# Performance work log

Hardware: AMD Instinct MI355X
Metric: run time of the kernel (lower is better)

Reference implementation:

```python
import jax, jax.numpy as jnp
import numpy as np

N_OFFSETS = [(1, 0), (1, 1), (0, 1), (-1, 1), (-1, 0), (-1, -1), (0, -1), (1, -1)]
DILATION = 1


def setup_inputs() -> dict:
    key = jax.random.key(0)
    feats = jax.random.normal(key, (8, 128, 256, 256), dtype=jnp.float32)
    return {"feats": feats}


def reference(feats):
    # feats: [B, C, H, W]
    d = DILATION
    B, C, H, W = feats.shape
    # channel-wise L2 normalize (no eps, matching torch .norm division)
    normed = feats / jnp.linalg.norm(feats, axis=1, keepdims=True)
    # reflect pad last two spatial dims by d
    padded = jnp.pad(normed, ((0, 0), (0, 0), (d, d), (d, d)), mode="reflect")
    # 8 shifted multiply + channel-sum correlations (fixed small offset set)
    corrs = jnp.concatenate(
        [
            jnp.sum(
                normed
                * padded[:, :, d - dx * d // d if False else d - dx:H + d - dx, d - dy:W + d - dy],
                axis=1,
                keepdims=True,
            )
            for dx, dy in [(ox * d, oy * d) for ox, oy in N_OFFSETS]
        ],
        axis=1,
    )  # [B, 8, H, W]
    return corrs
```

## Files before the change

kernel.cpp:

```cpp
#include <hip/hip_runtime.h>


#define BB 8
#define CC 128
#define HH 256
#define WW 256
#define CSPLIT 2
#define CPW (CC / CSPLIT)

#define DD(k, j) acc[12 + (k)*4 + (j)]

__global__ __launch_bounds__(128) void featcorr_kernel(
    const float* __restrict__ feats, float* __restrict__ out) {
  const int lane = threadIdx.x;
  const int wy = threadIdx.y;
  const int h = (blockIdx.x % 8) * (HH / 8) + (blockIdx.x / 8);
  const int b = blockIdx.y;

  const int hm = (h == 0) ? 1 : h - 1;
  const int hp = (h == HH - 1) ? HH - 2 : h + 1;

  const size_t HW = (size_t)HH * WW;
  const int col0 = lane * 4;

  const float* pT = feats + ((size_t)b * CC + wy * CPW) * HW + (size_t)hm * WW + col0;
  const float* pM = feats + ((size_t)b * CC + wy * CPW) * HW + (size_t)h * WW + col0;
  const float* pB = feats + ((size_t)b * CC + wy * CPW) * HW + (size_t)hp * WW + col0;

  float acc[44];
#pragma unroll
  for (int a = 0; a < 44; ++a) acc[a] = 0.f;

  auto compute = [&](const float4 t, const float4 m, const float4 bt) {
    const float rT = __shfl_down(t.x, 1);
    const float rM = __shfl_down(m.x, 1);
    const float rB = __shfl_down(bt.x, 1);
    acc[0] += t.x * t.x;  acc[1] += t.y * t.y;  acc[2] += t.z * t.z;  acc[3] += t.w * t.w;
    acc[4] += m.x * m.x;  acc[5] += m.y * m.y;  acc[6] += m.z * m.z;  acc[7] += m.w * m.w;
    acc[8] += bt.x * bt.x; acc[9] += bt.y * bt.y; acc[10] += bt.z * bt.z; acc[11] += bt.w * bt.w;
    DD(0, 0) += m.x * t.x; DD(0, 1) += m.y * t.y; DD(0, 2) += m.z * t.z; DD(0, 3) += m.w * t.w;
    DD(4, 0) += m.x * bt.x; DD(4, 1) += m.y * bt.y; DD(4, 2) += m.z * bt.z; DD(4, 3) += m.w * bt.w;
    DD(1, 1) += m.y * t.x; DD(1, 2) += m.z * t.y; DD(1, 3) += m.w * t.z;
    DD(1, 0) += rM * t.w;
    DD(2, 1) += m.y * m.x; DD(2, 2) += m.z * m.y; DD(2, 3) += m.w * m.z;
    DD(3, 1) += m.y * bt.x; DD(3, 2) += m.z * bt.y; DD(3, 3) += m.w * bt.z;
    DD(3, 0) += rM * bt.w;
    DD(5, 0) += m.x * bt.y; DD(5, 1) += m.y * bt.z; DD(5, 2) += m.z * bt.w; DD(5, 3) += m.w * rB;
    DD(6, 0) += m.x * m.y; DD(6, 1) += m.y * m.z; DD(6, 2) += m.z * m.w; DD(6, 3) += m.w * rM;
    DD(7, 0) += m.x * t.y; DD(7, 1) += m.y * t.z; DD(7, 2) += m.z * t.w; DD(7, 3) += m.w * rT;
  };

#define LOADSTEP(T, M, Bv)        \
  T = *(const float4*)pT;         \
  M = *(const float4*)pM;         \
  Bv = *(const float4*)pB;        \
  pT += HW; pM += HW; pB += HW;

  float4 tA, mA, bA, tB, mB, bB, tC, mC, bC, tD, mD, bD;
  LOADSTEP(tA, mA, bA)
  LOADSTEP(tB, mB, bB)
  LOADSTEP(tC, mC, bC)

  for (int i = 0; i < CPW / 4 - 1; ++i) {
    LOADSTEP(tD, mD, bD) compute(tA, mA, bA);
    LOADSTEP(tA, mA, bA) compute(tB, mB, bB);
    LOADSTEP(tB, mB, bB) compute(tC, mC, bC);
    LOADSTEP(tC, mC, bC) compute(tD, mD, bD);
  }
  LOADSTEP(tD, mD, bD) compute(tA, mA, bA);
  compute(tB, mB, bB);
  compute(tC, mC, bC);
  compute(tD, mD, bD);

  __shared__ float lds[44][64];
  if (wy == 1) {
#pragma unroll
    for (int a = 0; a < 44; ++a) lds[a][lane] = acc[a];
  }
  __syncthreads();

  if (wy == 0) {
#pragma unroll
    for (int a = 0; a < 44; ++a) acc[a] += lds[a][lane];

    const float g1 = __shfl_up(DD(1, 0), 1);
    const float g2 = __shfl_up(DD(6, 3), 1);
    const float g3 = __shfl_up(DD(3, 0), 1);
    DD(1, 0) = (lane == 0) ? DD(7, 0) : g1;
    DD(2, 0) = (lane == 0) ? DD(6, 0) : g2;
    DD(3, 0) = (lane == 0) ? DD(5, 0) : g3;
    if (lane == 63) {
      DD(5, 3) = DD(3, 3);
      DD(6, 3) = DD(2, 3);
      DD(7, 3) = DD(1, 3);
    }

    float it[4], im[4], ib[4];
#pragma unroll
    for (int j = 0; j < 4; ++j) {
      it[j] = rsqrtf(acc[j]);
      im[j] = rsqrtf(acc[4 + j]);
      ib[j] = rsqrtf(acc[8 + j]);
    }
    float IT[6], IM[6], IB[6];
    IT[1] = it[0]; IT[2] = it[1]; IT[3] = it[2]; IT[4] = it[3];
    IM[1] = im[0]; IM[2] = im[1]; IM[3] = im[2]; IM[4] = im[3];
    IB[1] = ib[0]; IB[2] = ib[1]; IB[3] = ib[2]; IB[4] = ib[3];
    const float tl = __shfl_up(it[3], 1), ml = __shfl_up(im[3], 1), bl = __shfl_up(ib[3], 1);
    const float tr = __shfl_down(it[0], 1), mr = __shfl_down(im[0], 1), br = __shfl_down(ib[0], 1);
    IT[0] = (lane == 0) ? it[1] : tl;
    IM[0] = (lane == 0) ? im[1] : ml;
    IB[0] = (lane == 0) ? ib[1] : bl;
    IT[5] = (lane == 63) ? it[2] : tr;
    IM[5] = (lane == 63) ? im[2] : mr;
    IB[5] = (lane == 63) ? ib[2] : br;

    float* obase = out + ((size_t)b * 8) * HW + (size_t)h * WW + col0;
#pragma unroll
    for (int k = 0; k < 8; ++k) {
      float v[4];
#pragma unroll
      for (int j = 0; j < 4; ++j) {
        float in;
        switch (k) {
          case 0: in = it[j];     break;
          case 1: in = IT[j];     break;
          case 2: in = IM[j];     break;
          case 3: in = IB[j];     break;
          case 4: in = ib[j];     break;
          case 5: in = IB[j + 2]; break;
          case 6: in = IM[j + 2]; break;
          default: in = IT[j + 2]; break;
        }
        v[j] = DD(k, j) * im[j] * in;
      }
      float4 o;
      o.x = v[0]; o.y = v[1]; o.z = v[2]; o.w = v[3];
      *(float4*)(obase + (size_t)k * HW) = o;
    }
  }
}

extern "C" void kernel_launch(void* const* d_in, const int* in_sizes, int n_in,
                              void* d_out, int out_size, void* d_ws, size_t ws_size,
                              hipStream_t stream) {
  const float* feats = (const float*)d_in[0];
  float* out = (float*)d_out;
  dim3 block(64, CSPLIT, 1);
  dim3 grid(HH, BB, 1);
  featcorr_kernel<<<grid, block, 0, stream>>>(feats, out);
}
```

Measured before the change: 365.2 us.

## Share row halos across warps via async global-to-LDS multi-buffered pipeline

Each block now handles 4 output rows with one warp per row. The 6 needed input rows per channel are staged into LDS with global_load_lds, using a 10-deep ring buffer controlled by manual vmcnt waits and barriers. The old design split channels across two warps and had each warp load 3 rows directly, so every input row was fetched about three times. Sharing rows across warps cuts that redundant global traffic and removes the cross-warp reduction, at the cost of two barriers per channel and a large LDS footprint (60KB) that limits occupancy.

```diff
diff --git a/kernel.cpp b/kernel.cpp
--- a/kernel.cpp
+++ b/kernel.cpp
@@ -5,33 +5,57 @@
 #define CC 128
 #define HH 256
 #define WW 256
-#define CSPLIT 2
-#define CPW (CC / CSPLIT)
+#define RB 4
+#define NSLOT 6
+#define PD 10
 
 #define DD(k, j) acc[12 + (k)*4 + (j)]
 
-__global__ __launch_bounds__(128) void featcorr_kernel(
+__global__ __launch_bounds__(256) void featcorr_kernel(
     const float* __restrict__ feats, float* __restrict__ out) {
   const int lane = threadIdx.x;
   const int wy = threadIdx.y;
-  const int h = (blockIdx.x % 8) * (HH / 8) + (blockIdx.x / 8);
+  const int rb = blockIdx.x;
   const int b = blockIdx.y;
-
-  const int hm = (h == 0) ? 1 : h - 1;
-  const int hp = (h == HH - 1) ? HH - 2 : h + 1;
+  const int h0 = rb * RB;
+  const int h = h0 + wy;
 
   const size_t HW = (size_t)HH * WW;
   const int col0 = lane * 4;
 
-  const float* pT = feats + ((size_t)b * CC + wy * CPW) * HW + (size_t)hm * WW + col0;
-  const float* pM = feats + ((size_t)b * CC + wy * CPW) * HW + (size_t)h * WW + col0;
-  const float* pB = feats + ((size_t)b * CC + wy * CPW) * HW + (size_t)hp * WW + col0;
+  __shared__ float lds[PD][NSLOT][WW];
+
+  const int hh1 = h0 - 1 + wy;
+  const int sr1 = (hh1 < 0) ? 1 : (hh1 > HH - 1 ? HH - 2 : hh1);
+  const float* p1 = feats + (size_t)b * CC * HW + (size_t)sr1 * WW + col0;
+  const float* p2 = nullptr;
+  if (wy < 2) {
+    const int hh2 = h0 - 1 + (4 + wy);
+    const int sr2 = (hh2 < 0) ? 1 : (hh2 > HH - 1 ? HH - 2 : hh2);
+    p2 = feats + (size_t)b * CC * HW + (size_t)sr2 * WW + col0;
+  }
+
+  auto stage = [&](int buf) {
+    __builtin_amdgcn_global_load_lds(
+        (const __attribute__((address_space(1))) void*)p1,
+        (__attribute__((address_space(3))) void*)&lds[buf][wy][0], 16, 0, 0);
+    p1 += HW;
+    if (wy < 2) {
+      __builtin_amdgcn_global_load_lds(
+          (const __attribute__((address_space(1))) void*)p2,
+          (__attribute__((address_space(3))) void*)&lds[buf][4 + wy][0], 16, 0, 0);
+      p2 += HW;
+    }
+  };
 
   float acc[44];
 #pragma unroll
   for (int a = 0; a < 44; ++a) acc[a] = 0.f;
 
-  auto compute = [&](const float4 t, const float4 m, const float4 bt) {
+  auto compute = [&](int buf) {
+    const float4 t = *(const float4*)&lds[buf][wy][col0];
+    const float4 m = *(const float4*)&lds[buf][wy + 1][col0];
+    const float4 bt = *(const float4*)&lds[buf][wy + 2][col0];
     const float rT = __shfl_down(t.x, 1);
     const float rM = __shfl_down(m.x, 1);
     const float rB = __shfl_down(bt.x, 1);
@@ -50,94 +74,82 @@
     DD(7, 0) += m.x * t.y; DD(7, 1) += m.y * t.z; DD(7, 2) += m.z * t.w; DD(7, 3) += m.w * rT;
   };
 
-#define LOADSTEP(T, M, Bv)        \
-  T = *(const float4*)pT;         \
-  M = *(const float4*)pM;         \
-  Bv = *(const float4*)pB;        \
-  pT += HW; pM += HW; pB += HW;
+#pragma unroll
+  for (int c = 0; c < PD; ++c) stage(c);
 
-  float4 tA, mA, bA, tB, mB, bB, tC, mC, bC, tD, mD, bD;
-  LOADSTEP(tA, mA, bA)
-  LOADSTEP(tB, mB, bB)
-  LOADSTEP(tC, mC, bC)
+  int buf = 0;
+  for (int ch = 0; ch < CC; ++ch) {
+    if (ch < CC - (PD - 1)) {
+      if (wy < 2) {
+        asm volatile("s_waitcnt vmcnt(18)" ::: "memory");
+      } else {
+        asm volatile("s_waitcnt vmcnt(9)" ::: "memory");
+      }
+    } else {
+      asm volatile("s_waitcnt vmcnt(0)" ::: "memory");
+    }
+    asm volatile("s_barrier" ::: "memory");
+    compute(buf);
+    asm volatile("s_waitcnt lgkmcnt(0)" ::: "memory");
+    asm volatile("s_barrier" ::: "memory");
+    if (ch + PD < CC) stage(buf);
+    buf = (buf + 1 == PD) ? 0 : buf + 1;
+  }
 
-  for (int i = 0; i < CPW / 4 - 1; ++i) {
-    LOADSTEP(tD, mD, bD) compute(tA, mA, bA);
-    LOADSTEP(tA, mA, bA) compute(tB, mB, bB);
-    LOADSTEP(tB, mB, bB) compute(tC, mC, bC);
-    LOADSTEP(tC, mC, bC) compute(tD, mD, bD);
+  const float g1 = __shfl_up(DD(1, 0), 1);
+  const float g2 = __shfl_up(DD(6, 3), 1);
+  const float g3 = __shfl_up(DD(3, 0), 1);
+  DD(1, 0) = (lane == 0) ? DD(7, 0) : g1;
+  DD(2, 0) = (lane == 0) ? DD(6, 0) : g2;
+  DD(3, 0) = (lane == 0) ? DD(5, 0) : g3;
+  if (lane == 63) {
+    DD(5, 3) = DD(3, 3);
+    DD(6, 3) = DD(2, 3);
+    DD(7, 3) = DD(1, 3);
   }
-  LOADSTEP(tD, mD, bD) compute(tA, mA, bA);
-  compute(tB, mB, bB);
-  compute(tC, mC, bC);
-  compute(tD, mD, bD);
 
-  __shared__ float lds[44][64];
-  if (wy == 1) {
+  float it[4], im[4], ib[4];
 #pragma unroll
-    for (int a = 0; a < 44; ++a) lds[a][lane] = acc[a];
+  for (int j = 0; j < 4; ++j) {
+    it[j] = rsqrtf(acc[j]);
+    im[j] = rsqrtf(acc[4 + j]);
+    ib[j] = rsqrtf(acc[8 + j]);
   }
-  __syncthreads();
+  float IT[6], IM[6], IB[6];
+  IT[1] = it[0]; IT[2] = it[1]; IT[3] = it[2]; IT[4] = it[3];
+  IM[1] = im[0]; IM[2] = im[1]; IM[3] = im[2]; IM[4] = im[3];
+  IB[1] = ib[0]; IB[2] = ib[1]; IB[3] = ib[2]; IB[4] = ib[3];
+  const float tl = __shfl_up(it[3], 1), ml = __shfl_up(im[3], 1), bl = __shfl_up(ib[3], 1);
+  const float tr = __shfl_down(it[0], 1), mr = __shfl_down(im[0], 1), br = __shfl_down(ib[0], 1);
+  IT[0] = (lane == 0) ? it[1] : tl;
+  IM[0] = (lane == 0) ? im[1] : ml;
+  IB[0] = (lane == 0) ? ib[1] : bl;
+  IT[5] = (lane == 63) ? it[2] : tr;
+  IM[5] = (lane == 63) ? im[2] : mr;
+  IB[5] = (lane == 63) ? ib[2] : br;
 
-  if (wy == 0) {
+  float* obase = out + ((size_t)b * 8) * HW + (size_t)h * WW + col0;
 #pragma unroll
-    for (int a = 0; a < 44; ++a) acc[a] += lds[a][lane];
-
-    const float g1 = __shfl_up(DD(1, 0), 1);
-    const float g2 = __shfl_up(DD(6, 3), 1);
-    const float g3 = __shfl_up(DD(3, 0), 1);
-    DD(1, 0) = (lane == 0) ? DD(7, 0) : g1;
-    DD(2, 0) = (lane == 0) ? DD(6, 0) : g2;
-    DD(3, 0) = (lane == 0) ? DD(5, 0) : g3;
-    if (lane == 63) {
-      DD(5, 3) = DD(3, 3);
-      DD(6, 3) = DD(2, 3);
-      DD(7, 3) = DD(1, 3);
-    }
-
-    float it[4], im[4], ib[4];
+  for (int k = 0; k < 8; ++k) {
+    float v[4];
 #pragma unroll
     for (int j = 0; j < 4; ++j) {
-      it[j] = rsqrtf(acc[j]);
-      im[j] = rsqrtf(acc[4 + j]);
-      ib[j] = rsqrtf(acc[8 + j]);
+      float in;
+      switch (k) {
+        case 0: in = it[j];     break;
+        case 1: in = IT[j];     break;
+        case 2: in = IM[j];     break;
+        case 3: in = IB[j];     break;
+        case 4: in = ib[j];     break;
+        case 5: in = IB[j + 2]; break;
+        case 6: in = IM[j + 2]; break;
+        default: in = IT[j + 2]; break;
+      }
+      v[j] = DD(k, j) * im[j] * in;
     }
-    float IT[6], IM[6], IB[6];
-    IT[1] = it[0]; IT[2] = it[1]; IT[3] = it[2]; IT[4] = it[3];
-    IM[1] = im[0]; IM[2] = im[1]; IM[3] = im[2]; IM[4] = im[3];
-    IB[1] = ib[0]; IB[2] = ib[1]; IB[3] = ib[2]; IB[4] = ib[3];
-    const float tl = __shfl_up(it[3], 1), ml = __shfl_up(im[3], 1), bl = __shfl_up(ib[3], 1);
-    const float tr = __shfl_down(it[0], 1), mr = __shfl_down(im[0], 1), br = __shfl_down(ib[0], 1);
-    IT[0] = (lane == 0) ? it[1] : tl;
-    IM[0] = (lane == 0) ? im[1] : ml;
-    IB[0] = (lane == 0) ? ib[1] : bl;
-    IT[5] = (lane == 63) ? it[2] : tr;
-    IM[5] = (lane == 63) ? im[2] : mr;
-    IB[5] = (lane == 63) ? ib[2] : br;
-
-    float* obase = out + ((size_t)b * 8) * HW + (size_t)h * WW + col0;
-#pragma unroll
-    for (int k = 0; k < 8; ++k) {
-      float v[4];
-#pragma unroll
-      for (int j = 0; j < 4; ++j) {
-        float in;
-        switch (k) {
-          case 0: in = it[j];     break;
-          case 1: in = IT[j];     break;
-          case 2: in = IM[j];     break;
-          case 3: in = IB[j];     break;
-          case 4: in = ib[j];     break;
-          case 5: in = IB[j + 2]; break;
-          case 6: in = IM[j + 2]; break;
-          default: in = IT[j + 2]; break;
-        }
-        v[j] = DD(k, j) * im[j] * in;
-      }
-      float4 o;
-      o.x = v[0]; o.y = v[1]; o.z = v[2]; o.w = v[3];
-      *(float4*)(obase + (size_t)k * HW) = o;
-    }
+    float4 o;
+    o.x = v[0]; o.y = v[1]; o.z = v[2]; o.w = v[3];
+    *(float4*)(obase + (size_t)k * HW) = o;
   }
 }
 
@@ -146,7 +158,7 @@
                               hipStream_t stream) {
   const float* feats = (const float*)d_in[0];
   float* out = (float*)d_out;
-  dim3 block(64, CSPLIT, 1);
-  dim3 grid(HH, BB, 1);
+  dim3 block(64, RB, 1);
+  dim3 grid(HH / RB, BB, 1);
   featcorr_kernel<<<grid, block, 0, stream>>>(feats, out);
 }
```

Result: no change. 370.1 us (+1.3%).
